# Kernel tuning notes

Hardware: AMD Instinct MI355X
Metric: run time of the kernel (lower is better)

## Reference

```python
import jax, jax.numpy as jnp
import numpy as np

B, C, H, W = 16, 512, 64, 64


def setup_inputs() -> dict:
    key = jax.random.key(0)
    ks = jax.random.split(key, 8)
    s = 1.0 / np.sqrt(C)  # fan-in scale like torch conv default
    return {
        "x": jax.random.normal(ks[0], (B, C, H, W), dtype=jnp.float32),
        "y": jax.random.normal(ks[1], (B, C), dtype=jnp.float32),
        "wq": jax.random.normal(ks[2], (C, C), dtype=jnp.float32) * s,
        "bq": jax.random.normal(ks[3], (C,), dtype=jnp.float32) * s,
        "wk": jax.random.normal(ks[4], (C, C), dtype=jnp.float32) * s,
        "bk": jax.random.normal(ks[5], (C,), dtype=jnp.float32) * s,
        "wv": jax.random.normal(ks[6], (C, C), dtype=jnp.float32) * s,
        "bv": jax.random.normal(ks[7], (C,), dtype=jnp.float32) * s,
        "gamma": jnp.ones((1,), dtype=jnp.float32),
    }


def _conv1x1_flat(inp_flat, w, b):
    # inp_flat: (B, C, N); 1x1 conv == per-pixel channel GEMM
    return jnp.einsum("oc,bcn->bon", w, inp_flat) + b[None, :, None]


def reference(x, y, wq, bq, wk, bk, wv, bv, gamma):
    b, c, h, w = x.shape
    n = h * w
    # align=True: y (B, C) broadcast to (B, C, H, W); flatten spatial dims
    y_flat = jnp.broadcast_to(y[:, :, None], (b, c, n))
    x_flat = x.reshape(b, c, n)
    # exchange=False: q = y, k = v = x
    pq = _conv1x1_flat(y_flat, wq, bq)          # (B, C, N)
    pk = _conv1x1_flat(x_flat, wk, bk)          # (B, C, N)
    pv = _conv1x1_flat(x_flat, wv, bv)          # (B, C, N)
    energy = jnp.einsum("bcn,bdn->bcd", pq, pk)  # (B, C, C) channel attention
    attn = jax.nn.softmax(energy, axis=-1)
    out = jnp.einsum("bcd,bdn->bcn", attn, pv)   # (B, C, N)
    out = out.reshape(b, c, h, w)
    return gamma * out + x
```

## Files before the change

kernel.cpp:

```cpp
#include <hip/hip_runtime.h>
#include <hip/hip_bf16.h>

#define Bn 16
#define Cn 512
#define Nn 4096

typedef unsigned short u16;
typedef __bf16 bf16x8 __attribute__((ext_vector_type(8)));
typedef float f32x4 __attribute__((ext_vector_type(4)));
typedef unsigned short u16x8 __attribute__((ext_vector_type(8)));

__device__ __forceinline__ u16 f2bf(float f) {
    __hip_bfloat16 h = __float2bfloat16(f);
    return *reinterpret_cast<u16*>(&h);
}

__device__ __forceinline__ void glds16(const u16* g, u16* l) {
    __builtin_amdgcn_global_load_lds(
        (const __attribute__((address_space(1))) void*)g,
        (__attribute__((address_space(3))) void*)l, 16, 0, 0);
}

__global__ __launch_bounds__(256) void k_transpose(
    const float* __restrict__ x, u16* __restrict__ xt, float* __restrict__ sxp)
{
    __shared__ float tile[128 * 65];
    const int b = blockIdx.z, c0 = blockIdx.y * 128, n0 = blockIdx.x * 64;
    const int t = threadIdx.x;
    const float* xb = x + ((size_t)(b * Cn + c0)) * Nn + n0;

    float part[8];
#pragma unroll
    for (int r = 0; r < 8; ++r) {
        int cl = (t >> 4) + r * 16;
        int nl = (t & 15) * 4;
        float4 v = *(const float4*)(xb + (size_t)cl * Nn + nl);
        float* tp = &tile[cl * 65 + nl];
        tp[0] = v.x; tp[1] = v.y; tp[2] = v.z; tp[3] = v.w;
        part[r] = (v.x + v.y) + (v.z + v.w);
    }
#pragma unroll
    for (int m = 1; m < 16; m <<= 1) {
#pragma unroll
        for (int r = 0; r < 8; ++r) part[r] += __shfl_xor(part[r], m);
    }
    if ((t & 15) == 0) {
#pragma unroll
        for (int r = 0; r < 8; ++r) {
            int cl = (t >> 4) + r * 16;
            sxp[(size_t)(b * Cn + c0 + cl) * 64 + blockIdx.x] = part[r];
        }
    }
    __syncthreads();
    u16* xtb = xt + ((size_t)(b * Nn + n0)) * Cn + c0;
#pragma unroll
    for (int r = 0; r < 4; ++r) {
        int nl = (t >> 4) + r * 16;
        int c8 = (t & 15) * 8;
        u16x8 hv;
#pragma unroll
        for (int i = 0; i < 8; ++i) hv[i] = f2bf(tile[(c8 + i) * 65 + nl]);
        *(u16x8*)(xtb + (size_t)nl * Cn + c8) = hv;
    }
}

__global__ __launch_bounds__(256) void k_sxred(
    const float* __restrict__ sxp, float* __restrict__ sx)
{
    int i = blockIdx.x * 256 + threadIdx.x;
    const float4* p = (const float4*)(sxp + (size_t)i * 64);
    float s = 0.f;
#pragma unroll
    for (int j = 0; j < 16; ++j) {
        float4 v = p[j];
        s += (v.x + v.y) + (v.z + v.w);
    }
    sx[i] = s;
}

__global__ __launch_bounds__(256) void k_qk(
    const float* __restrict__ wq, const float* __restrict__ bq,
    const float* __restrict__ wk, const float* __restrict__ bk,
    const float* __restrict__ y, const float* __restrict__ sx,
    float* __restrict__ qy, float* __restrict__ sk)
{
    const int w = threadIdx.x >> 6, lane = threadIdx.x & 63;
    const int o = blockIdx.x * 4 + w;
    const int b = blockIdx.y;
    const int mode = blockIdx.z;
    const float* W = mode ? wk : wq;
    const float* vec = mode ? (sx + b * Cn) : (y + b * Cn);
    float sum = 0.f;
#pragma unroll
    for (int i = 0; i < 8; ++i) {
        int k2 = lane + i * 64;
        sum += W[(size_t)o * Cn + k2] * vec[k2];
    }
#pragma unroll
    for (int m = 1; m < 64; m <<= 1) sum += __shfl_xor(sum, m);
    if (lane == 0) {
        if (mode) sk[b * Cn + o] = sum + 4096.0f * bk[o];
        else      qy[b * Cn + o] = sum + bq[o];
    }
}

__global__ __launch_bounds__(256) void k_wvt(
    const float* __restrict__ wv, u16* __restrict__ wvt)
{
    __shared__ float tl[64 * 65];
    const int d0 = blockIdx.x * 64, e0 = blockIdx.y * 64;
    const int t = threadIdx.x;
#pragma unroll
    for (int r = 0; r < 4; ++r) {
        int d = (t >> 4) + r * 16, e4 = (t & 15) * 4;
        float4 v = *(const float4*)(wv + (size_t)(d0 + d) * Cn + e0 + e4);
        float* p = &tl[d * 65 + e4];
        p[0] = v.x; p[1] = v.y; p[2] = v.z; p[3] = v.w;
    }
    __syncthreads();
#pragma unroll
    for (int r = 0; r < 4; ++r) {
        int e = (t >> 4) + r * 16, d4 = (t & 15) * 4;
        ushort4 h;
        h.x = f2bf(tl[(d4 + 0) * 65 + e]);
        h.y = f2bf(tl[(d4 + 1) * 65 + e]);
        h.z = f2bf(tl[(d4 + 2) * 65 + e]);
        h.w = f2bf(tl[(d4 + 3) * 65 + e]);
        *(ushort4*)(wvt + (size_t)(e0 + e) * Cn + d0 + d4) = h;
    }
}

__global__ __launch_bounds__(256) void k_softmax(
    const float* __restrict__ qy, const float* __restrict__ sk,
    const float* __restrict__ bv, u16* __restrict__ attn,
    float* __restrict__ beff)
{
    __shared__ float red[4], red2[4], red3[4];
    const int b = blockIdx.x >> 9, c = blockIdx.x & 511;
    const int t = threadIdx.x;
    const float q = qy[b * Cn + c];
    const float l0 = q * sk[b * Cn + t];
    const float l1 = q * sk[b * Cn + t + 256];
    float mx = fmaxf(l0, l1);
#pragma unroll
    for (int m = 1; m < 64; m <<= 1) mx = fmaxf(mx, __shfl_xor(mx, m));
    if ((t & 63) == 0) red[t >> 6] = mx;
    __syncthreads();
    mx = fmaxf(fmaxf(red[0], red[1]), fmaxf(red[2], red[3]));
    const float e0 = __expf(l0 - mx), e1 = __expf(l1 - mx);
    float s = e0 + e1;
#pragma unroll
    for (int m = 1; m < 64; m <<= 1) s += __shfl_xor(s, m);
    if ((t & 63) == 0) red2[t >> 6] = s;
    __syncthreads();
    s = red2[0] + red2[1] + red2[2] + red2[3];
    const float inv = 1.0f / s;
    const float a0 = e0 * inv, a1 = e1 * inv;
    u16* arow = attn + ((size_t)(b * Cn + c)) * Cn;
    arow[t] = f2bf(a0);
    arow[t + 256] = f2bf(a1);
    float pb = a0 * bv[t] + a1 * bv[t + 256];
#pragma unroll
    for (int m = 1; m < 64; m <<= 1) pb += __shfl_xor(pb, m);
    if ((t & 63) == 0) red3[t >> 6] = pb;
    __syncthreads();
    if (t == 0) beff[b * Cn + c] = red3[0] + red3[1] + red3[2] + red3[3];
}

template <int FINAL>
__global__ __launch_bounds__(256) void k_gemm(
    const u16* __restrict__ A, size_t strideA,
    const u16* __restrict__ Bt, size_t strideB,
    int N,
    u16* __restrict__ outBf, size_t strideOb,
    float* __restrict__ outF,
    const float* __restrict__ xres,
    const float* __restrict__ beff,
    const float* __restrict__ gamma)
{
    constexpr int K = 512;
    __shared__ float smem_f[8448];
    u16* la = (u16*)smem_f;
    u16* lb = la + 128 * 64;
    const int b = blockIdx.z;
    const int m0 = blockIdx.y * 128;
    const int n0 = blockIdx.x * 128;
    A  += (size_t)b * strideA;
    Bt += (size_t)b * strideB;
    const int t = threadIdx.x;
    const int lane = t & 63;
    const int w = t >> 6;
    const int wm = (w >> 1) * 64, wn = (w & 1) * 64;
    const int l15 = lane & 15, quad = lane >> 4;

    f32x4 acc[4][4];
#pragma unroll
    for (int i = 0; i < 4; ++i)
#pragma unroll
        for (int j = 0; j < 4; ++j)
            acc[i][j] = (f32x4){0.f, 0.f, 0.f, 0.f};

    const int srow8 = lane >> 3;
    const int lgcol = ((lane & 7) ^ srow8) * 8;

    for (int k0 = 0; k0 < K; k0 += 64) {
        __syncthreads();
#pragma unroll
        for (int j = 0; j < 4; ++j) {
            const int row = w * 32 + j * 8 + srow8;
            const int sb = (w * 256 + j * 64) * 8;
            glds16(A  + (size_t)(m0 + row) * K + k0 + lgcol, la + sb);
            glds16(Bt + (size_t)(n0 + row) * K + k0 + lgcol, lb + sb);
        }
        __syncthreads();

#pragma unroll
        for (int kk2 = 0; kk2 < 2; ++kk2) {
            bf16x8 af[4], bfr[4];
#pragma unroll
            for (int mi = 0; mi < 4; ++mi) {
                const int r = wm + mi * 16 + l15;
                const int pg = ((kk2 << 2) + quad) ^ (l15 & 7);
                af[mi] = *(const bf16x8*)&la[r * 64 + pg * 8];
            }
#pragma unroll
            for (int ni = 0; ni < 4; ++ni) {
                const int r = wn + ni * 16 + l15;
                const int pg = ((kk2 << 2) + quad) ^ (l15 & 7);
                bfr[ni] = *(const bf16x8*)&lb[r * 64 + pg * 8];
            }
#pragma unroll
            for (int mi = 0; mi < 4; ++mi)
#pragma unroll
                for (int ni = 0; ni < 4; ++ni)
                    acc[mi][ni] = __builtin_amdgcn_mfma_f32_16x16x32_bf16(
                        af[mi], bfr[ni], acc[mi][ni], 0, 0, 0);
        }
    }

    if (FINAL) {
        const float g = gamma[0];
        float* lc = smem_f;
#pragma unroll
        for (int h = 0; h < 2; ++h) {
            __syncthreads();
            if ((w >> 1) == h) {
#pragma unroll
                for (int mi = 0; mi < 4; ++mi)
#pragma unroll
                    for (int reg = 0; reg < 4; ++reg) {
                        const int rl = mi * 16 + quad * 4 + reg;
#pragma unroll
                        for (int ni = 0; ni < 4; ++ni)
                            lc[rl * 132 + wn + ni * 16 + l15] = acc[mi][ni][reg];
                    }
            }
            __syncthreads();
            const int rb = h * 64;
#pragma unroll
            for (int rr = 0; rr < 8; ++rr) {
                const int rl = rr * 8 + (t >> 5);
                const int c4 = (t & 31) * 4;
                float4 v = *(float4*)&lc[rl * 132 + c4];
                const int r = m0 + rb + rl;
                const float be = beff[b * Cn + r];
                const size_t base = ((size_t)(b * Cn + r)) * N + n0 + c4;
                float4 xr = *(const float4*)(xres + base);
                float4 o;
                o.x = g * (v.x + be) + xr.x;
                o.y = g * (v.y + be) + xr.y;
                o.z = g * (v.z + be) + xr.z;
                o.w = g * (v.w + be) + xr.w;
                *(float4*)(outF + base) = o;
            }
        }
    } else {
#pragma unroll
        for (int mi = 0; mi < 4; ++mi) {
#pragma unroll
            for (int reg = 0; reg < 4; ++reg) {
                const int r = m0 + wm + mi * 16 + quad * 4 + reg;
                const size_t base = (size_t)b * strideOb + (size_t)r * N;
#pragma unroll
                for (int ni = 0; ni < 4; ++ni) {
                    const int cidx = n0 + wn + ni * 16 + l15;
                    outBf[base + cidx] = f2bf(acc[mi][ni][reg]);
                }
            }
        }
    }
}

extern "C" void kernel_launch(void* const* d_in, const int* in_sizes, int n_in,
                              void* d_out, int out_size, void* d_ws, size_t ws_size,
                              hipStream_t stream)
{
    const float* x     = (const float*)d_in[0];
    const float* y     = (const float*)d_in[1];
    const float* wq    = (const float*)d_in[2];
    const float* bq    = (const float*)d_in[3];
    const float* wk    = (const float*)d_in[4];
    const float* bk    = (const float*)d_in[5];
    const float* wv    = (const float*)d_in[6];
    const float* bv    = (const float*)d_in[7];
    const float* gamma = (const float*)d_in[8];
    float* out = (float*)d_out;

    char* ws = (char*)d_ws;
    u16*   xt   = (u16*)  (ws + 0);
    float* sxp  = (float*)(ws + 67108864);
    float* sx   = (float*)(ws + 69206016);
    float* qy   = (float*)(ws + 69238784);
    float* sk   = (float*)(ws + 69271552);
    float* beff = (float*)(ws + 69304320);
    u16*   attn = (u16*)  (ws + 69337088);
    u16*   wvt  = (u16*)  (ws + 77725696);
    u16*   weff = (u16*)  (ws + 78249984);

    k_transpose<<<dim3(64, 4, Bn), dim3(256), 0, stream>>>(x, xt, sxp);
    k_sxred<<<dim3(32), dim3(256), 0, stream>>>(sxp, sx);
    k_wvt<<<dim3(8, 8), dim3(256), 0, stream>>>(wv, wvt);
    k_qk<<<dim3(128, Bn, 2), dim3(256), 0, stream>>>(wq, bq, wk, bk, y, sx, qy, sk);
    k_softmax<<<dim3(Bn * Cn), dim3(256), 0, stream>>>(qy, sk, bv, attn, beff);
    k_gemm<0><<<dim3(4, 4, Bn), dim3(256), 0, stream>>>(
        attn, (size_t)Cn * Cn, wvt, (size_t)0, Cn,
        weff, (size_t)Cn * Cn, nullptr, nullptr, nullptr, nullptr);
    k_gemm<1><<<dim3(32, 4, Bn), dim3(256), 0, stream>>>(
        weff, (size_t)Cn * Cn, xt, (size_t)Nn * Cn, Nn,
        nullptr, (size_t)0, out, x, beff, gamma);
}
```

Baseline: 352.6 us.

## Replace final GEMM with 256x256-tile, 512-thread double-buffered MFMA kernel

Adds a new final GEMM kernel (weff times xt plus residual epilogue) that uses 256x256 output tiles, 8 waves, and 128 KB of dynamic LDS double-buffering with async global-to-LDS loads. The loads are interleaved with MFMA phases using barriers and setprio. The epilogue stages accumulators through LDS so the output and residual reads and writes use coalesced float4. The aim is more data reuse per loaded tile and overlap of memory traffic with matrix math in the dominant GEMM. In exchange, the large LDS footprint limits occupancy to one block per CU, and the grid shrinks to 512 blocks.

```diff
diff --git a/kernel.cpp b/kernel.cpp
--- a/kernel.cpp
+++ b/kernel.cpp
@@ -291,6 +291,154 @@
     }
 }
 
+#define FRAG(tp, row, gg) \
+    (*(const bf16x8*)&(tp)[(row) * 64 + (((gg) ^ ((row) & 7)) << 3)])
+#define MFMA16(base)                                                          \
+    {                                                                         \
+        _Pragma("unroll") for (int mi = 0; mi < 4; ++mi) {                    \
+            _Pragma("unroll") for (int ni = 0; ni < 4; ++ni)                  \
+                acc[(base) + mi][ni] =                                        \
+                    __builtin_amdgcn_mfma_f32_16x16x32_bf16(                  \
+                        af[mi], bf[ni], acc[(base) + mi][ni], 0, 0, 0);       \
+        }                                                                     \
+    }
+
+__global__ __launch_bounds__(512) void k_gemm2(
+    const u16* __restrict__ A,
+    const u16* __restrict__ Bt,
+    float* __restrict__ outF,
+    const float* __restrict__ xres,
+    const float* __restrict__ beff,
+    const float* __restrict__ gamma)
+{
+    extern __shared__ u16 sm[];
+    u16* ab = sm;
+    u16* bb = sm + 32768;
+    const int b = blockIdx.z;
+    const int m0 = blockIdx.y << 8;
+    const int n0 = blockIdx.x << 8;
+    const int t = threadIdx.x;
+    const int lane = t & 63, w = t >> 6;
+    const int wm = (w >> 2) << 7, wn = (w & 3) << 6;
+    const int l15 = lane & 15, quad = lane >> 4;
+
+    const u16* Ag = A + (size_t)b * Cn * Cn;
+    const u16* Bg = Bt + (size_t)b * ((size_t)Nn * Cn);
+    const int srow = t >> 3;
+    const int scol = ((t & 7) ^ (srow & 7)) << 3;
+    const u16* pa = Ag + (size_t)(m0 + srow) * Cn + scol;
+    const u16* pb = Bg + (size_t)(n0 + srow) * Cn + scol;
+    u16* da = ab + w * 512;
+    u16* db = bb + w * 512;
+
+#define STG_A(q, c, kk) \
+    glds16(pa + (size_t)(c) * (64 * Cn) + (kk), da + (q) * 16384 + (c) * 4096)
+#define STG_B(q, c, kk) \
+    glds16(pb + (size_t)(c) * (64 * Cn) + (kk), db + (q) * 16384 + (c) * 4096)
+
+    f32x4 acc[8][4];
+#pragma unroll
+    for (int i = 0; i < 8; ++i)
+#pragma unroll
+        for (int j = 0; j < 4; ++j) acc[i][j] = (f32x4){0.f, 0.f, 0.f, 0.f};
+
+    STG_A(0, 0, 0); STG_A(0, 2, 0); STG_B(0, 0, 0); STG_B(0, 1, 0);
+    STG_B(0, 2, 0); STG_B(0, 3, 0); STG_A(0, 1, 0); STG_A(0, 3, 0);
+    asm volatile("s_waitcnt vmcnt(2)" ::: "memory");
+    __builtin_amdgcn_s_barrier();
+
+    for (int tI = 0; tI < 8; ++tI) {
+        const int q = tI & 1, nq = q ^ 1;
+        const int kn = (tI + 1) << 6;
+        const u16* ca = ab + q * 16384;
+        const u16* cb = bb + q * 16384;
+        const bool st = (tI < 7);
+        bf16x8 af[4], bf[4];
+
+#pragma unroll
+        for (int mi = 0; mi < 4; ++mi) af[mi] = FRAG(ca, wm + mi * 16 + l15, quad);
+#pragma unroll
+        for (int ni = 0; ni < 4; ++ni) bf[ni] = FRAG(cb, wn + ni * 16 + l15, quad);
+        if (st) { STG_A(nq, 0, kn); STG_A(nq, 2, kn); STG_B(nq, 0, kn); STG_B(nq, 1, kn); }
+        __builtin_amdgcn_s_barrier();
+        __builtin_amdgcn_s_setprio(1);
+        MFMA16(0)
+        __builtin_amdgcn_s_setprio(0);
+        if (st) { asm volatile("s_waitcnt vmcnt(4)" ::: "memory"); }
+        else    { asm volatile("s_waitcnt vmcnt(0)" ::: "memory"); }
+        __builtin_amdgcn_s_barrier();
+
+#pragma unroll
+        for (int mi = 0; mi < 4; ++mi) af[mi] = FRAG(ca, wm + 64 + mi * 16 + l15, quad);
+        if (st) { STG_B(nq, 2, kn); STG_B(nq, 3, kn); }
+        __builtin_amdgcn_s_barrier();
+        __builtin_amdgcn_s_setprio(1);
+        MFMA16(4)
+        __builtin_amdgcn_s_setprio(0);
+        __builtin_amdgcn_s_barrier();
+
+#pragma unroll
+        for (int mi = 0; mi < 4; ++mi) af[mi] = FRAG(ca, wm + mi * 16 + l15, 4 + quad);
+#pragma unroll
+        for (int ni = 0; ni < 4; ++ni) bf[ni] = FRAG(cb, wn + ni * 16 + l15, 4 + quad);
+        if (st) { STG_A(nq, 1, kn); STG_A(nq, 3, kn); }
+        __builtin_amdgcn_s_barrier();
+        __builtin_amdgcn_s_setprio(1);
+        MFMA16(0)
+        __builtin_amdgcn_s_setprio(0);
+        __builtin_amdgcn_s_barrier();
+
+#pragma unroll
+        for (int mi = 0; mi < 4; ++mi) af[mi] = FRAG(ca, wm + 64 + mi * 16 + l15, 4 + quad);
+        __builtin_amdgcn_s_barrier();
+        __builtin_amdgcn_s_setprio(1);
+        MFMA16(4)
+        __builtin_amdgcn_s_setprio(0);
+        if (st) { asm volatile("s_waitcnt vmcnt(2)" ::: "memory"); }
+        __builtin_amdgcn_s_barrier();
+    }
+
+    __syncthreads();
+    float* lc = (float*)sm;
+    const float gmv = gamma[0];
+#pragma unroll
+    for (int h = 0; h < 4; ++h) {
+        if (h) __syncthreads();
+        if ((w >> 2) == (h >> 1)) {
+            const int qm = h & 1;
+#pragma unroll
+            for (int mi = 0; mi < 4; ++mi)
+#pragma unroll
+                for (int reg = 0; reg < 4; ++reg) {
+                    const int rl = mi * 16 + quad * 4 + reg;
+#pragma unroll
+                    for (int ni = 0; ni < 4; ++ni)
+                        lc[rl * 260 + wn + ni * 16 + l15] = acc[qm * 4 + mi][ni][reg];
+                }
+        }
+        __syncthreads();
+#pragma unroll
+        for (int k = 0; k < 8; ++k) {
+            const int r = w + k * 8;
+            const int row = m0 + h * 64 + r;
+            float4 v = *(float4*)&lc[r * 260 + (t & 63) * 4];
+            const float be = beff[b * Cn + row];
+            const size_t base = ((size_t)(b * Cn + row)) * Nn + n0 + (t & 63) * 4;
+            float4 xr = *(const float4*)(xres + base);
+            float4 o;
+            o.x = gmv * (v.x + be) + xr.x;
+            o.y = gmv * (v.y + be) + xr.y;
+            o.z = gmv * (v.z + be) + xr.z;
+            o.w = gmv * (v.w + be) + xr.w;
+            *(float4*)(outF + base) = o;
+        }
+    }
+#undef STG_A
+#undef STG_B
+}
+#undef FRAG
+#undef MFMA16
+
 extern "C" void kernel_launch(void* const* d_in, const int* in_sizes, int n_in,
                               void* d_out, int out_size, void* d_ws, size_t ws_size,
                               hipStream_t stream)
@@ -325,7 +473,14 @@
     k_gemm<0><<<dim3(4, 4, Bn), dim3(256), 0, stream>>>(
         attn, (size_t)Cn * Cn, wvt, (size_t)0, Cn,
         weff, (size_t)Cn * Cn, nullptr, nullptr, nullptr, nullptr);
-    k_gemm<1><<<dim3(32, 4, Bn), dim3(256), 0, stream>>>(
-        weff, (size_t)Cn * Cn, xt, (size_t)Nn * Cn, Nn,
-        nullptr, (size_t)0, out, x, beff, gamma);
-}
+    if (hipFuncSetAttribute((const void*)k_gemm2,
+                            hipFuncAttributeMaxDynamicSharedMemorySize,
+                            131072) == hipSuccess) {
+        k_gemm2<<<dim3(Nn / 256, 2, Bn), dim3(512), 131072, stream>>>(
+            weff, xt, out, x, beff, gamma);
+    } else {
+        k_gemm<1><<<dim3(32, 4, Bn), dim3(256), 0, stream>>>(
+            weff, (size_t)Cn * Cn, xt, (size_t)Nn * Cn, Nn,
+            nullptr, (size_t)0, out, x, beff, gamma);
+    }
+}
```

After: 355.5 us. Within noise of the previous version (+0.8%).

## Add 256x128-tile triple-buffered GEMM with LDS-staged coalesced epilogue for final projection

Applied to the files above, without the earlier changes.

Replaces the final weff×xt GEMM with a new kernel using 512-thread blocks, 256x128 output tiles, and a three-stage global_load_lds pipeline with XOR-swizzled shared memory. The epilogue stages accumulators through LDS so the residual add and bias are written with coalesced float4 stores. This aims to improve operand reuse, overlap loads with MFMA, and fix poorly coalesced output writes. It costs 72KB of dynamic LDS, which limits occupancy, and it falls back to the old kernel if that attribute cannot be set.

```diff
diff --git a/kernel.cpp b/kernel.cpp
--- a/kernel.cpp
+++ b/kernel.cpp
@@ -291,6 +291,117 @@
     }
 }
 
+__global__ __launch_bounds__(512, 4) void k_gemm2(
+    const u16* __restrict__ A,
+    const u16* __restrict__ Bt,
+    float* __restrict__ outF,
+    const float* __restrict__ xres,
+    const float* __restrict__ beff,
+    const float* __restrict__ gamma)
+{
+    extern __shared__ u16 sm[];
+    const int b = blockIdx.z;
+    const int m0 = blockIdx.y << 8;
+    const int n0 = blockIdx.x << 7;
+    const int t = threadIdx.x;
+    const int lane = t & 63, w = t >> 6;
+    const int wm = (w >> 1) << 6, wn = (w & 1) << 6;
+    const int l15 = lane & 15, quad = lane >> 4;
+
+    const u16* Ag = A + (size_t)b * Cn * Cn;
+    const u16* Bg = Bt + (size_t)b * ((size_t)Nn * Cn);
+    const int srow = t >> 2;
+    const int scol = (((t & 3) ^ ((srow >> 1) & 3))) << 3;
+    const u16* pa = Ag + (size_t)(m0 + srow) * Cn + scol;
+    const u16* pb = Bg + (size_t)(n0 + srow) * Cn + scol;
+    u16* dw = sm + w * 512;
+
+#define SLOTO(s) ((s) * 12288)
+#define STGA(s, c, k0) \
+    glds16(pa + (size_t)(c) * (128 * Cn) + (k0), dw + SLOTO(s) + (c) * 4096)
+#define STGB(s, k0) glds16(pb + (k0), dw + SLOTO(s) + 8192)
+#define FRG(base, row, qd) \
+    (*(const bf16x8*)&sm[(base) + (row) * 32 + \
+                         (((qd) ^ (((row) >> 1) & 3)) << 3)])
+
+    f32x4 acc[4][4];
+#pragma unroll
+    for (int i = 0; i < 4; ++i)
+#pragma unroll
+        for (int j = 0; j < 4; ++j) acc[i][j] = (f32x4){0.f, 0.f, 0.f, 0.f};
+
+    STGA(0, 0, 0); STGA(0, 1, 0); STGB(0, 0);
+    STGA(1, 0, 32); STGA(1, 1, 32); STGB(1, 32);
+
+#pragma unroll
+    for (int tI = 0; tI < 16; ++tI) {
+        if (tI < 15) { asm volatile("s_waitcnt vmcnt(3)" ::: "memory"); }
+        else         { asm volatile("s_waitcnt vmcnt(0)" ::: "memory"); }
+        __builtin_amdgcn_s_barrier();
+        if (tI <= 13) {
+            const int s2 = (tI + 2) % 3;
+            const int k2 = (tI + 2) << 5;
+            STGA(s2, 0, k2); STGA(s2, 1, k2); STGB(s2, k2);
+        }
+        const int sb = SLOTO(tI % 3);
+        bf16x8 af[4], bf[4];
+#pragma unroll
+        for (int mi = 0; mi < 4; ++mi)
+            af[mi] = FRG(sb, wm + mi * 16 + l15, quad);
+#pragma unroll
+        for (int ni = 0; ni < 4; ++ni)
+            bf[ni] = FRG(sb + 8192, wn + ni * 16 + l15, quad);
+        __builtin_amdgcn_s_setprio(1);
+#pragma unroll
+        for (int mi = 0; mi < 4; ++mi)
+#pragma unroll
+            for (int ni = 0; ni < 4; ++ni)
+                acc[mi][ni] = __builtin_amdgcn_mfma_f32_16x16x32_bf16(
+                    af[mi], bf[ni], acc[mi][ni], 0, 0, 0);
+        __builtin_amdgcn_s_setprio(0);
+    }
+#undef STGA
+#undef STGB
+#undef FRG
+#undef SLOTO
+
+    __syncthreads();
+    float* lc = (float*)sm;
+    const float g = gamma[0];
+#pragma unroll
+    for (int h = 0; h < 4; ++h) {
+        if (h) __syncthreads();
+        if ((w >> 1) == h) {
+#pragma unroll
+            for (int mi = 0; mi < 4; ++mi)
+#pragma unroll
+                for (int reg = 0; reg < 4; ++reg) {
+                    const int rl = mi * 16 + quad * 4 + reg;
+#pragma unroll
+                    for (int ni = 0; ni < 4; ++ni)
+                        lc[rl * 132 + wn + ni * 16 + l15] = acc[mi][ni][reg];
+                }
+        }
+        __syncthreads();
+#pragma unroll
+        for (int k = 0; k < 4; ++k) {
+            const int r = (t >> 5) + k * 16;
+            const int c4 = (t & 31) * 4;
+            float4 v = *(float4*)&lc[r * 132 + c4];
+            const int row = m0 + h * 64 + r;
+            const float be = beff[b * Cn + row];
+            const size_t base = ((size_t)(b * Cn + row)) * Nn + n0 + c4;
+            float4 xr = *(const float4*)(xres + base);
+            float4 o;
+            o.x = g * (v.x + be) + xr.x;
+            o.y = g * (v.y + be) + xr.y;
+            o.z = g * (v.z + be) + xr.z;
+            o.w = g * (v.w + be) + xr.w;
+            *(float4*)(outF + base) = o;
+        }
+    }
+}
+
 extern "C" void kernel_launch(void* const* d_in, const int* in_sizes, int n_in,
                               void* d_out, int out_size, void* d_ws, size_t ws_size,
                               hipStream_t stream)
@@ -325,7 +436,14 @@
     k_gemm<0><<<dim3(4, 4, Bn), dim3(256), 0, stream>>>(
         attn, (size_t)Cn * Cn, wvt, (size_t)0, Cn,
         weff, (size_t)Cn * Cn, nullptr, nullptr, nullptr, nullptr);
-    k_gemm<1><<<dim3(32, 4, Bn), dim3(256), 0, stream>>>(
-        weff, (size_t)Cn * Cn, xt, (size_t)Nn * Cn, Nn,
-        nullptr, (size_t)0, out, x, beff, gamma);
-}
+    if (hipFuncSetAttribute((const void*)k_gemm2,
+                            hipFuncAttributeMaxDynamicSharedMemorySize,
+                            73728) == hipSuccess) {
+        k_gemm2<<<dim3(Nn / 128, 2, Bn), dim3(512), 73728, stream>>>(
+            weff, xt, out, x, beff, gamma);
+    } else {
+        k_gemm<1><<<dim3(32, 4, Bn), dim3(256), 0, stream>>>(
+            weff, (size_t)Cn * Cn, xt, (size_t)Nn * Cn, Nn,
+            nullptr, (size_t)0, out, x, beff, gamma);
+    }
+}
```

Measured after the change: 346.6 us. No clear change (-1.7%).
